# Kernel tuning notes

Measured on AMD Instinct MI355X. Metric: run time of the kernel, lower is better.

Reference implementation:

```python
import jax, jax.numpy as jnp
import numpy as np

DIM = 512
HEADS = 8
HD = DIM // HEADS
WS = 4          # window_size
SHIFT = 2       # window_size // 2
HID = 4 * DIM   # mlp hidden
EPS = 1e-5


def _ln(x, g, b):
    m = jnp.mean(x, axis=-1, keepdims=True)
    v = jnp.mean((x - m) ** 2, axis=-1, keepdims=True)
    return (x - m) * jax.lax.rsqrt(v + EPS) * g + b


def setup_inputs() -> dict:
    key = jax.random.key(0)
    ks = jax.random.split(key, 12)
    s = 0.02
    return {
        "x": jax.random.normal(ks[0], (2, 32, 32, 32, DIM), dtype=jnp.float32),
        "ln1_g": jnp.ones((DIM,), jnp.float32),
        "ln1_b": jnp.zeros((DIM,), jnp.float32),
        "qkv_w": jax.random.normal(ks[1], (DIM, 3 * DIM), jnp.float32) * s,
        "qkv_b": jnp.zeros((3 * DIM,), jnp.float32),
        "proj_w": jax.random.normal(ks[2], (DIM, DIM), jnp.float32) * s,
        "proj_b": jnp.zeros((DIM,), jnp.float32),
        "ln2_g": jnp.ones((DIM,), jnp.float32),
        "ln2_b": jnp.zeros((DIM,), jnp.float32),
        "ffn_w1": jax.random.normal(ks[3], (DIM, HID), jnp.float32) * s,
        "ffn_b1": jnp.zeros((HID,), jnp.float32),
        "ffn_w2": jax.random.normal(ks[4], (HID, DIM), jnp.float32) * s,
        "ffn_b2": jnp.zeros((DIM,), jnp.float32),
    }


def reference(x, ln1_g, ln1_b, qkv_w, qkv_b, proj_w, proj_b,
              ln2_g, ln2_b, ffn_w1, ffn_b1, ffn_w2, ffn_b2):
    B, D, H, W, C = x.shape
    nD, nH, nW = D // WS, H // WS, W // WS
    N = WS ** 3

    # cyclic shift
    xs = jnp.roll(x, (-SHIFT, -SHIFT, -SHIFT), axis=(1, 2, 3))

    # window partition: (B*numWin, N, C)
    xw = xs.reshape(B, nD, WS, nH, WS, nW, WS, C)
    xw = xw.transpose(0, 1, 3, 5, 2, 4, 6, 7).reshape(-1, N, C)

    # pre-norm attention
    h = _ln(xw, ln1_g, ln1_b)
    qkv = (h @ qkv_w + qkv_b).reshape(-1, N, 3, HEADS, HD)
    q, k, v = jnp.moveaxis(qkv, 2, 0)          # each (Bn, N, HEADS, HD)
    scale = HD ** -0.5
    logits = jnp.einsum('bnhd,bmhd->bhnm', q, k) * scale
    attn = jax.nn.softmax(logits, axis=-1)
    out = jnp.einsum('bhnm,bmhd->bnhd', attn, v).reshape(-1, N, C)
    out = out @ proj_w + proj_b
    xw = xw + out

    # window reverse + unshift
    xo = xw.reshape(B, nD, nH, nW, WS, WS, WS, C)
    xo = xo.transpose(0, 1, 4, 2, 5, 3, 6, 7).reshape(B, D, H, W, C)
    xo = jnp.roll(xo, (SHIFT, SHIFT, SHIFT), axis=(1, 2, 3))

    # pre-norm FFN (exact GELU, dropout inactive in eval)
    h2 = _ln(xo, ln2_g, ln2_b)
    ffn = jax.nn.gelu(h2 @ ffn_w1 + ffn_b1, approximate=False) @ ffn_w2 + ffn_b2
    return xo + ffn
```

## Files before the change

kernel.cpp:

```cpp
#include <hip/hip_runtime.h>
#include <hip/hip_bf16.h>


typedef __attribute__((ext_vector_type(4))) short short4v;
typedef __attribute__((ext_vector_type(8))) short short8v;
typedef __attribute__((ext_vector_type(4))) float f32x4;

__device__ __forceinline__ unsigned short f2bf(float f) {
  unsigned u = __float_as_uint(f);
  u += 0x7fffu + ((u >> 16) & 1u);
  return (unsigned short)(u >> 16);
}

__device__ __forceinline__ void gload_lds16(const unsigned short* g, unsigned short* l) {
  __builtin_amdgcn_global_load_lds(
      (const __attribute__((address_space(1))) unsigned int*)g,
      (__attribute__((address_space(3))) unsigned int*)l, 16, 0, 0);
}

__global__ __launch_bounds__(256)
void wprep_kernel(const float* __restrict__ w, unsigned short* __restrict__ wt,
                  int kbits, int total, int N) {
  int idx = blockIdx.x * 256 + threadIdx.x;
  if (idx >= total) return;
  int K = 1 << kbits;
  int n = idx >> kbits, kk = idx & (K - 1);
  wt[idx] = f2bf(w[(long)kk * N + n]);
}

__global__ __launch_bounds__(256)
void ln_kernel(const float* __restrict__ src, const float* __restrict__ g,
               const float* __restrict__ bb, unsigned short* __restrict__ dst,
               const int gather) {
  const int lane = threadIdx.x & 63;
  const int row = blockIdx.x * 4 + (threadIdx.x >> 6);
  long srow;
  if (gather) {
    int n = row & 63, win = row >> 6;
    int w0 = win & 7, h0 = (win >> 3) & 7, d0 = (win >> 6) & 7, b2 = win >> 9;
    int dx = n & 3, dy = (n >> 2) & 3, dz = n >> 4;
    int od = (d0 * 4 + dz + 2) & 31, oh = (h0 * 4 + dy + 2) & 31, ow = (w0 * 4 + dx + 2) & 31;
    srow = (((long)b2 * 32 + od) * 32 + oh) * 32 + ow;
  } else {
    srow = row;
  }
  const float4* sp = (const float4*)(src + srow * 512);
  float4 x0 = sp[lane], x1 = sp[lane + 64];
  float sum = x0.x + x0.y + x0.z + x0.w + x1.x + x1.y + x1.z + x1.w;
  float sq  = x0.x*x0.x + x0.y*x0.y + x0.z*x0.z + x0.w*x0.w
            + x1.x*x1.x + x1.y*x1.y + x1.z*x1.z + x1.w*x1.w;
#pragma unroll
  for (int off = 1; off < 64; off <<= 1) {
    sum += __shfl_xor(sum, off, 64);
    sq  += __shfl_xor(sq, off, 64);
  }
  float mean = sum * (1.0f / 512.0f);
  float var  = sq * (1.0f / 512.0f) - mean * mean;
  float rstd = rsqrtf(var + 1e-5f);
  float4 g0 = ((const float4*)g)[lane], g1 = ((const float4*)g)[lane + 64];
  float4 b0 = ((const float4*)bb)[lane], b1v = ((const float4*)bb)[lane + 64];
  ushort4 o0, o1;
  o0.x = f2bf((x0.x - mean) * rstd * g0.x + b0.x);
  o0.y = f2bf((x0.y - mean) * rstd * g0.y + b0.y);
  o0.z = f2bf((x0.z - mean) * rstd * g0.z + b0.z);
  o0.w = f2bf((x0.w - mean) * rstd * g0.w + b0.w);
  o1.x = f2bf((x1.x - mean) * rstd * g1.x + b1v.x);
  o1.y = f2bf((x1.y - mean) * rstd * g1.y + b1v.y);
  o1.z = f2bf((x1.z - mean) * rstd * g1.z + b1v.z);
  o1.w = f2bf((x1.w - mean) * rstd * g1.w + b1v.w);
  *(ushort4*)(dst + (long)row * 512 + lane * 4) = o0;
  *(ushort4*)(dst + (long)row * 512 + 256 + lane * 4) = o1;
}

template <int EPI>
__global__ __launch_bounds__(256)
void gemm_bt(const unsigned short* __restrict__ A,
             const unsigned short* __restrict__ Bt,
             const float* __restrict__ bias, int K,
             void* __restrict__ out0,
             unsigned short* __restrict__ out1,
             unsigned short* __restrict__ out2,
             const float* __restrict__ res) {
  __shared__ unsigned short As[128 * 32];
  __shared__ unsigned short Bs[128 * 32];
  const int tid = threadIdx.x;
  const int lane = tid & 63;
  const int wv = tid >> 6;
  const int quad = lane >> 4;
  const int l15 = lane & 15;
  const int wm = (wv >> 1) << 6;
  const int wn = (wv & 1) << 6;
  const long row0 = (long)blockIdx.y * 128;
  const long col0 = (long)blockIdx.x * 128;

  f32x4 acc[4][4] = {};

  const int srw = lane >> 2;
  const int sch = lane & 3;

  for (int kk = 0; kk < K; kk += 32) {
    __syncthreads();
#pragma unroll
    for (int c = 0; c < 2; ++c) {
      const int r = c * 64 + wv * 16 + srw;
      const int gch = sch ^ ((r >> 1) & 3);
      gload_lds16(A + (row0 + r) * K + kk + gch * 8, &As[(c * 64 + wv * 16) * 32]);
      gload_lds16(Bt + (col0 + r) * K + kk + gch * 8, &Bs[(c * 64 + wv * 16) * 32]);
    }
    __syncthreads();
    short8v af[4], bf[4];
#pragma unroll
    for (int t = 0; t < 4; ++t) {
      const int ra = wm + t * 16 + l15;
      af[t] = *(const short8v*)&As[ra * 32 + (quad ^ ((ra >> 1) & 3)) * 8];
      const int rb = wn + t * 16 + l15;
      bf[t] = *(const short8v*)&Bs[rb * 32 + (quad ^ ((rb >> 1) & 3)) * 8];
    }
#pragma unroll
    for (int mt = 0; mt < 4; ++mt)
#pragma unroll
      for (int nt = 0; nt < 4; ++nt)
        acc[mt][nt] = __builtin_amdgcn_mfma_f32_16x16x32_bf16(af[mt], bf[nt], acc[mt][nt], 0, 0, 0);
  }

#pragma unroll
  for (int mt = 0; mt < 4; ++mt) {
#pragma unroll
    for (int nt = 0; nt < 4; ++nt) {
#pragma unroll
      for (int r = 0; r < 4; ++r) {
        const long gr = row0 + wm + mt * 16 + quad * 4 + r;
        const long gc = col0 + wn + nt * 16 + l15;
        float val = acc[mt][nt][r] + bias[gc];
        if (EPI == 0) {
          int which = (int)(gc >> 9), rem = (int)gc & 511;
          int head = rem >> 6, hd = rem & 63;
          long win = gr >> 6, n = gr & 63;
          long base = (win * 8 + head) * 4096;
          unsigned short bv = f2bf(val);
          if (which == 0)      ((unsigned short*)out0)[base + n * 64 + hd] = bv;
          else if (which == 1) out1[base + n * 64 + hd] = bv;
          else                 out2[base + hd * 64 + n] = bv;
        } else if (EPI == 1) {
          int win = (int)(gr >> 6), n = (int)gr & 63;
          int w0 = win & 7, h0 = (win >> 3) & 7, d0 = (win >> 6) & 7, b2 = win >> 9;
          int dx = n & 3, dy = (n >> 2) & 3, dz = n >> 4;
          int od = (d0 * 4 + dz + 2) & 31, oh = (h0 * 4 + dy + 2) & 31, ow = (w0 * 4 + dx + 2) & 31;
          long addr = ((((long)b2 * 32 + od) * 32 + oh) * 32 + ow) * 512 + gc;
          ((float*)out0)[addr] = res[addr] + val;
        } else if (EPI == 2) {
          float ge = 0.5f * val * (1.0f + erff(val * 0.70710678118654752f));
          ((unsigned short*)out0)[gr * 2048 + gc] = f2bf(ge);
        } else {
          long addr = gr * 512 + gc;
          ((float*)out0)[addr] = res[addr] + val;
        }
      }
    }
  }
}

__global__ __launch_bounds__(256)
void attn_kernel(const unsigned short* __restrict__ q,
                 const unsigned short* __restrict__ k,
                 const unsigned short* __restrict__ vt,
                 unsigned short* __restrict__ out) {
  __shared__ unsigned short Ps[4][64 * 72];
  const int lane = threadIdx.x & 63;
  const int wave = threadIdx.x >> 6;
  const int quad = lane >> 4;
  const int l15 = lane & 15;
  const int unit = blockIdx.x * 4 + wave;
  const int win = unit >> 3;
  const int head = unit & 7;
  const long base = (long)unit * 4096;

  f32x4 s[4][4] = {};
#pragma unroll
  for (int kk = 0; kk < 64; kk += 32) {
    short8v a[4], b[4];
#pragma unroll
    for (int t = 0; t < 4; ++t) {
      a[t] = *(const short8v*)(q + base + (t * 16 + l15) * 64 + kk + quad * 8);
      b[t] = *(const short8v*)(k + base + (t * 16 + l15) * 64 + kk + quad * 8);
    }
#pragma unroll
    for (int mt = 0; mt < 4; ++mt)
#pragma unroll
      for (int nt = 0; nt < 4; ++nt)
        s[mt][nt] = __builtin_amdgcn_mfma_f32_16x16x32_bf16(a[mt], b[nt], s[mt][nt], 0, 0, 0);
  }

  float lrow[4][4];
#pragma unroll
  for (int mt = 0; mt < 4; ++mt) {
#pragma unroll
    for (int r = 0; r < 4; ++r) {
      float v0 = s[mt][0][r] * 0.125f, v1 = s[mt][1][r] * 0.125f;
      float v2 = s[mt][2][r] * 0.125f, v3 = s[mt][3][r] * 0.125f;
      float mx = fmaxf(fmaxf(v0, v1), fmaxf(v2, v3));
#pragma unroll
      for (int off = 1; off < 16; off <<= 1) mx = fmaxf(mx, __shfl_xor(mx, off, 64));
      v0 = __expf(v0 - mx); v1 = __expf(v1 - mx);
      v2 = __expf(v2 - mx); v3 = __expf(v3 - mx);
      float sm = v0 + v1 + v2 + v3;
#pragma unroll
      for (int off = 1; off < 16; off <<= 1) sm += __shfl_xor(sm, off, 64);
      lrow[mt][r] = sm;
      int row = mt * 16 + quad * 4 + r;
      Ps[wave][row * 72 + 0 + l15]  = f2bf(v0);
      Ps[wave][row * 72 + 16 + l15] = f2bf(v1);
      Ps[wave][row * 72 + 32 + l15] = f2bf(v2);
      Ps[wave][row * 72 + 48 + l15] = f2bf(v3);
    }
  }
  __syncthreads();

  f32x4 o[4][4] = {};
#pragma unroll
  for (int kk = 0; kk < 64; kk += 32) {
    short8v a[4], b[4];
#pragma unroll
    for (int t = 0; t < 4; ++t) {
      a[t] = *(const short8v*)(&Ps[wave][(t * 16 + l15) * 72 + kk + quad * 8]);
      b[t] = *(const short8v*)(vt + base + (t * 16 + l15) * 64 + kk + quad * 8);
    }
#pragma unroll
    for (int mt = 0; mt < 4; ++mt)
#pragma unroll
      for (int nt = 0; nt < 4; ++nt)
        o[mt][nt] = __builtin_amdgcn_mfma_f32_16x16x32_bf16(a[mt], b[nt], o[mt][nt], 0, 0, 0);
  }

#pragma unroll
  for (int mt = 0; mt < 4; ++mt)
#pragma unroll
    for (int nt = 0; nt < 4; ++nt)
#pragma unroll
      for (int r = 0; r < 4; ++r) {
        int row = mt * 16 + quad * 4 + r;
        int col = nt * 16 + l15;
        float val = o[mt][nt][r] / lrow[mt][r];
        out[((long)win * 64 + row) * 512 + head * 64 + col] = f2bf(val);
      }
}

extern "C" void kernel_launch(void* const* d_in, const int* in_sizes, int n_in,
                              void* d_out, int out_size, void* d_ws, size_t ws_size,
                              hipStream_t stream) {
  const float* x      = (const float*)d_in[0];
  const float* ln1_g  = (const float*)d_in[1];
  const float* ln1_b  = (const float*)d_in[2];
  const float* qkv_w  = (const float*)d_in[3];
  const float* qkv_b  = (const float*)d_in[4];
  const float* proj_w = (const float*)d_in[5];
  const float* proj_b = (const float*)d_in[6];
  const float* ln2_g  = (const float*)d_in[7];
  const float* ln2_b  = (const float*)d_in[8];
  const float* w1     = (const float*)d_in[9];
  const float* b1     = (const float*)d_in[10];
  const float* w2     = (const float*)d_in[11];
  const float* b2     = (const float*)d_in[12];

  char* ws = (char*)d_ws;
  unsigned short* wt_qkv  = (unsigned short*)(ws + 0);
  unsigned short* wt_proj = (unsigned short*)(ws + 1572864);
  unsigned short* wt_1    = (unsigned short*)(ws + 2097152);
  unsigned short* wt_2    = (unsigned short*)(ws + 4194304);
  float*          xo      = (float*)(ws + 8388608);
  unsigned short* h       = (unsigned short*)(ws + 142606336);
  unsigned short* attno   = (unsigned short*)(ws + 209715200);
  unsigned short* qb      = (unsigned short*)(ws + 276824064);
  unsigned short* kb      = (unsigned short*)(ws + 343932928);
  unsigned short* vb      = (unsigned short*)(ws + 411041792);
  unsigned short* hid     = (unsigned short*)(ws + 209715200);
  float* out = (float*)d_out;

  wprep_kernel<<<3072, 256, 0, stream>>>(qkv_w, wt_qkv, 9, 512 * 1536, 1536);
  wprep_kernel<<<1024, 256, 0, stream>>>(proj_w, wt_proj, 9, 512 * 512, 512);
  wprep_kernel<<<4096, 256, 0, stream>>>(w1, wt_1, 9, 512 * 2048, 2048);
  wprep_kernel<<<4096, 256, 0, stream>>>(w2, wt_2, 11, 2048 * 512, 512);

  ln_kernel<<<16384, 256, 0, stream>>>(x, ln1_g, ln1_b, h, 1);
  gemm_bt<0><<<dim3(12, 512), 256, 0, stream>>>(h, wt_qkv, qkv_b, 512, qb, kb, vb, nullptr);
  attn_kernel<<<2048, 256, 0, stream>>>(qb, kb, vb, attno);
  gemm_bt<1><<<dim3(4, 512), 256, 0, stream>>>(attno, wt_proj, proj_b, 512, xo, nullptr, nullptr, x);
  ln_kernel<<<16384, 256, 0, stream>>>(xo, ln2_g, ln2_b, h, 0);
  gemm_bt<2><<<dim3(16, 512), 256, 0, stream>>>(h, wt_1, b1, 512, hid, nullptr, nullptr, nullptr);
  gemm_bt<3><<<dim3(4, 512), 256, 0, stream>>>(hid, wt_2, b2, 2048, out, nullptr, nullptr, xo);
}
```

Before: 1.208 ms.

## Double-buffer GEMM LDS tiles and merge weight-prep launches into one kernel

The GEMM main loop now uses two LDS buffers, so the async global-to-LDS loads for the next K-slice are issued while MFMAs run on the current slice. Global and LDS addresses are precomputed outside the loop. The four weight transpose/convert launches are merged into one kernel that picks its source by index range, which removes launch overhead. The extra buffers double the LDS per block, which could lower occupancy.

```diff
diff --git a/kernel.cpp b/kernel.cpp
--- a/kernel.cpp
+++ b/kernel.cpp
@@ -19,12 +19,18 @@
 }
 
 __global__ __launch_bounds__(256)
-void wprep_kernel(const float* __restrict__ w, unsigned short* __restrict__ wt,
-                  int kbits, int total, int N) {
+void wprep_all(const float* __restrict__ qkv_w, const float* __restrict__ proj_w,
+               const float* __restrict__ w1, const float* __restrict__ w2,
+               unsigned short* __restrict__ wt) {
   int idx = blockIdx.x * 256 + threadIdx.x;
-  if (idx >= total) return;
+  const float* w; int kbits, N, base;
+  if (idx < 786432)       { w = qkv_w;  kbits = 9;  N = 1536; base = 0; }
+  else if (idx < 1048576) { w = proj_w; kbits = 9;  N = 512;  base = 786432; }
+  else if (idx < 2097152) { w = w1;     kbits = 9;  N = 2048; base = 1048576; }
+  else                    { w = w2;     kbits = 11; N = 512;  base = 2097152; }
+  int li = idx - base;
   int K = 1 << kbits;
-  int n = idx >> kbits, kk = idx & (K - 1);
+  int n = li >> kbits, kk = li & (K - 1);
   wt[idx] = f2bf(w[(long)kk * N + n]);
 }
 
@@ -81,8 +87,8 @@
              unsigned short* __restrict__ out1,
              unsigned short* __restrict__ out2,
              const float* __restrict__ res) {
-  __shared__ unsigned short As[128 * 32];
-  __shared__ unsigned short Bs[128 * 32];
+  __shared__ unsigned short As0[128 * 32], Bs0[128 * 32];
+  __shared__ unsigned short As1[128 * 32], Bs1[128 * 32];
   const int tid = threadIdx.x;
   const int lane = tid & 63;
   const int wv = tid >> 6;
@@ -97,31 +103,55 @@
 
   const int srw = lane >> 2;
   const int sch = lane & 3;
-
-  for (int kk = 0; kk < K; kk += 32) {
+  const int r0 = wv * 16 + srw, r1 = 64 + wv * 16 + srw;
+  const unsigned short* gA0 = A  + (row0 + r0) * K + (sch ^ ((r0 >> 1) & 3)) * 8;
+  const unsigned short* gA1 = A  + (row0 + r1) * K + (sch ^ ((r1 >> 1) & 3)) * 8;
+  const unsigned short* gB0 = Bt + (col0 + r0) * K + (sch ^ ((r0 >> 1) & 3)) * 8;
+  const unsigned short* gB1 = Bt + (col0 + r1) * K + (sch ^ ((r1 >> 1) & 3)) * 8;
+  const int ld0 = (wv * 16) * 32, ld1 = (64 + wv * 16) * 32;
+
+  int offA[4], offB[4];
+#pragma unroll
+  for (int t = 0; t < 4; ++t) {
+    const int ra = wm + t * 16 + l15;
+    offA[t] = ra * 32 + (quad ^ ((ra >> 1) & 3)) * 8;
+    const int rb = wn + t * 16 + l15;
+    offB[t] = rb * 32 + (quad ^ ((rb >> 1) & 3)) * 8;
+  }
+
+#define STAGE(AS, BS, kkx) do {                    \
+    gload_lds16(gA0 + (kkx), &AS[ld0]);            \
+    gload_lds16(gB0 + (kkx), &BS[ld0]);            \
+    gload_lds16(gA1 + (kkx), &AS[ld1]);            \
+    gload_lds16(gB1 + (kkx), &BS[ld1]);            \
+  } while (0)
+
+#define COMPUTE(AS, BS) do {                                                   \
+    short8v af[4], bf[4];                                                      \
+    _Pragma("unroll")                                                          \
+    for (int t = 0; t < 4; ++t) {                                              \
+      af[t] = *(const short8v*)&AS[offA[t]];                                   \
+      bf[t] = *(const short8v*)&BS[offB[t]];                                   \
+    }                                                                          \
+    _Pragma("unroll")                                                          \
+    for (int mt = 0; mt < 4; ++mt)                                             \
+      _Pragma("unroll")                                                        \
+      for (int nt = 0; nt < 4; ++nt)                                           \
+        acc[mt][nt] = __builtin_amdgcn_mfma_f32_16x16x32_bf16(                 \
+            af[mt], bf[nt], acc[mt][nt], 0, 0, 0);                             \
+  } while (0)
+
+  STAGE(As0, Bs0, 0);
+  for (int kk = 0; kk < K; kk += 64) {
     __syncthreads();
-#pragma unroll
-    for (int c = 0; c < 2; ++c) {
-      const int r = c * 64 + wv * 16 + srw;
-      const int gch = sch ^ ((r >> 1) & 3);
-      gload_lds16(A + (row0 + r) * K + kk + gch * 8, &As[(c * 64 + wv * 16) * 32]);
-      gload_lds16(Bt + (col0 + r) * K + kk + gch * 8, &Bs[(c * 64 + wv * 16) * 32]);
-    }
+    STAGE(As1, Bs1, kk + 32);
+    COMPUTE(As0, Bs0);
     __syncthreads();
-    short8v af[4], bf[4];
-#pragma unroll
-    for (int t = 0; t < 4; ++t) {
-      const int ra = wm + t * 16 + l15;
-      af[t] = *(const short8v*)&As[ra * 32 + (quad ^ ((ra >> 1) & 3)) * 8];
-      const int rb = wn + t * 16 + l15;
-      bf[t] = *(const short8v*)&Bs[rb * 32 + (quad ^ ((rb >> 1) & 3)) * 8];
-    }
-#pragma unroll
-    for (int mt = 0; mt < 4; ++mt)
-#pragma unroll
-      for (int nt = 0; nt < 4; ++nt)
-        acc[mt][nt] = __builtin_amdgcn_mfma_f32_16x16x32_bf16(af[mt], bf[nt], acc[mt][nt], 0, 0, 0);
-  }
+    if (kk + 64 < K) STAGE(As0, Bs0, kk + 64);
+    COMPUTE(As1, Bs1);
+  }
+#undef STAGE
+#undef COMPUTE
 
 #pragma unroll
   for (int mt = 0; mt < 4; ++mt) {
@@ -263,6 +293,7 @@
   const float* b2     = (const float*)d_in[12];
 
   char* ws = (char*)d_ws;
+  unsigned short* wt_all  = (unsigned short*)ws;
   unsigned short* wt_qkv  = (unsigned short*)(ws + 0);
   unsigned short* wt_proj = (unsigned short*)(ws + 1572864);
   unsigned short* wt_1    = (unsigned short*)(ws + 2097152);
@@ -276,10 +307,7 @@
   unsigned short* hid     = (unsigned short*)(ws + 209715200);
   float* out = (float*)d_out;
 
-  wprep_kernel<<<3072, 256, 0, stream>>>(qkv_w, wt_qkv, 9, 512 * 1536, 1536);
-  wprep_kernel<<<1024, 256, 0, stream>>>(proj_w, wt_proj, 9, 512 * 512, 512);
-  wprep_kernel<<<4096, 256, 0, stream>>>(w1, wt_1, 9, 512 * 2048, 2048);
-  wprep_kernel<<<4096, 256, 0, stream>>>(w2, wt_2, 11, 2048 * 512, 512);
+  wprep_all<<<12288, 256, 0, stream>>>(qkv_w, proj_w, w1, w2, wt_all);
 
   ln_kernel<<<16384, 256, 0, stream>>>(x, ln1_g, ln1_b, h, 1);
   gemm_bt<0><<<dim3(12, 512), 256, 0, stream>>>(h, wt_qkv, qkv_b, 512, qb, kb, vb, nullptr);
```

Result: faster. 1.160 ms (-4.0%).
